# Kernel tuning notes

Hardware: AMD Instinct MI355X
Metric: run time of the kernel (lower is better)

The kernel has to match this reference:

```python
import jax, jax.numpy as jnp
import numpy as np

SIGMA = 100.0
M = 64
N_DIMS = 3
XH_IN = 9           # n_dims + in_node_nf + context_node_nf
XH_HID = 64         # xh_hidden_size
POS_HID = 192       # hidden_size - xh_hidden_size
TWO_PI = 2.0 * np.pi


def setup_inputs() -> dict:
    key = jax.random.key(0)
    ks = jax.random.split(key, 6)
    B, N = 8, 256
    t = jax.random.uniform(ks[0], (B, 1), dtype=jnp.float32)
    xh = jax.random.normal(ks[1], (B, N, XH_IN), dtype=jnp.float32)
    node_mask = jnp.ones((B, N, 1), dtype=jnp.float32)
    edge_mask = jnp.ones((B, N * N, 1), dtype=jnp.float32)
    # learned params: xh_embedder Linear(9->64), pos_embedder Linear(2m->192)
    W_xh = jax.random.normal(ks[2], (XH_IN, XH_HID), dtype=jnp.float32) / np.sqrt(XH_IN)
    b_xh = jnp.zeros((XH_HID,), dtype=jnp.float32)
    W_pos = jax.random.normal(ks[3], (2 * M, POS_HID), dtype=jnp.float32) / np.sqrt(2 * M)
    b_pos = jnp.zeros((POS_HID,), dtype=jnp.float32)
    return {"t": t, "xh": xh, "node_mask": node_mask, "edge_mask": edge_mask,
            "W_xh": W_xh, "b_xh": b_xh, "W_pos": W_pos, "b_pos": b_pos}


def remove_mean_with_mask(x, node_mask, N):
    # masked mean over node axis, re-masked output
    mean = jnp.sum(x * node_mask, axis=1, keepdims=True) / N  # [B,1,3]
    return (x - mean) * node_mask


def positional_encoding(d, sigma, m):
    # d: [B,N,N,1] -> Fourier features [B,N,N,2m] with geometric freqs sigma^(j/m)
    freqs = sigma ** (jnp.arange(m, dtype=jnp.float32) / m)  # [m]
    ang = TWO_PI * d * freqs                                  # [B,N,N,m]
    return jnp.concatenate([jnp.sin(ang), jnp.cos(ang)], axis=-1)


def reference(t, xh, node_mask, edge_mask, W_xh, b_xh, W_pos, b_pos):
    x = xh[..., :N_DIMS]
    h = xh[..., N_DIMS:]
    N = jnp.sum(node_mask, axis=1, keepdims=True)  # [B,1,1]
    x = remove_mean_with_mask(x, node_mask, N)
    # node feature embedding: [B,N,64]
    xh_emb = jnp.concatenate([x, h], axis=-1) @ W_xh + b_xh
    # pairwise distances (safe sqrt for diagonal zeros)
    diff = x[:, :, None, :] - x[:, None, :, :]                 # [B,N,N,3]
    sq = jnp.maximum(jnp.sum(diff * diff, axis=-1), 0.0)
    dist = jnp.sqrt(sq + 1e-12)                                # [B,N,N]
    pe = positional_encoding(dist[..., None], SIGMA, M)        # [B,N,N,2m]
    pe = pe * node_mask[:, :, :, None] * node_mask[:, None, :, :]
    pe = (pe @ W_pos + b_pos)                                  # [B,N,N,192]
    pe = jnp.sum(pe, axis=-2) / N                              # [B,N,192]
    out = jnp.concatenate([xh_emb, pe], axis=-1) * node_mask   # [B,N,256]
    return out
```

## Files before the change

### kernel.cpp

```cpp
#include <hip/hip_runtime.h>
#include <math.h>

#define BB 8
#define NN 256
#define XHIN 9
#define XHHID 64
#define POSHID 192

__global__ __launch_bounds__(256) void emb_center_kernel(
    const float* __restrict__ xh, const float* __restrict__ mask,
    const float* __restrict__ Wxh, const float* __restrict__ bxh,
    float* __restrict__ out, float* __restrict__ ws_xc, float* __restrict__ ws_cnt)
{
  const int b = blockIdx.x;
  const int n = threadIdx.x;

  const float* p = xh + (b * NN + n) * XHIN;
  float v[XHIN];
  #pragma unroll
  for (int k = 0; k < XHIN; ++k) v[k] = p[k];
  const float m = mask[b * NN + n];

  float a0 = v[0] * m, a1 = v[1] * m, a2 = v[2] * m, a3 = m;
  #pragma unroll
  for (int off = 32; off > 0; off >>= 1) {
    a0 += __shfl_down(a0, off, 64);
    a1 += __shfl_down(a1, off, 64);
    a2 += __shfl_down(a2, off, 64);
    a3 += __shfl_down(a3, off, 64);
  }
  __shared__ float red[4][4];
  __shared__ float Wl[XHIN * XHHID];
  __shared__ float bl[XHHID];
  const int lane = n & 63, wv = n >> 6;
  if (lane == 0) { red[wv][0] = a0; red[wv][1] = a1; red[wv][2] = a2; red[wv][3] = a3; }
  for (int idx = n; idx < XHIN * XHHID; idx += 256) Wl[idx] = Wxh[idx];
  if (n < XHHID) bl[n] = bxh[n];
  __syncthreads();

  const float s0 = red[0][0] + red[1][0] + red[2][0] + red[3][0];
  const float s1 = red[0][1] + red[1][1] + red[2][1] + red[3][1];
  const float s2 = red[0][2] + red[1][2] + red[2][2] + red[3][2];
  const float cnt = red[0][3] + red[1][3] + red[2][3] + red[3][3];
  const float inv = 1.0f / cnt;

  v[0] = (v[0] - s0 * inv) * m;
  v[1] = (v[1] - s1 * inv) * m;
  v[2] = (v[2] - s2 * inv) * m;

  ws_xc[(b * 3 + 0) * NN + n] = v[0];
  ws_xc[(b * 3 + 1) * NN + n] = v[1];
  ws_xc[(b * 3 + 2) * NN + n] = v[2];
  if (n == 0) ws_cnt[b] = cnt;

  float* o = out + (size_t)(b * NN + n) * 256;
  for (int oo = 0; oo < XHHID; ++oo) {
    float acc = bl[oo];
    #pragma unroll
    for (int k = 0; k < XHIN; ++k) acc = fmaf(v[k], Wl[k * XHHID + oo], acc);
    o[oo] = acc * m;
  }
}

__global__ __launch_bounds__(256) void pe_kernel(
    const float* __restrict__ ws_xc, const float* __restrict__ ws_cnt,
    const float* __restrict__ mask, const float* __restrict__ Wp,
    const float* __restrict__ bp, float* __restrict__ out)
{
  const int blk = blockIdx.x;
  const int b = blk >> 8;
  const int i = blk & 255;
  const int tid = threadIdx.x;

  __shared__ float dist_s[NN];
  __shared__ float mask_s[NN];
  __shared__ float part[4][128];
  __shared__ float Ssc[128];

  const float* xcb = ws_xc + b * 3 * NN;
  const float xi0 = xcb[0 * NN + i];
  const float xi1 = xcb[1 * NN + i];
  const float xi2 = xcb[2 * NN + i];
  {
    const int j = tid;
    const float dx = xi0 - xcb[0 * NN + j];
    const float dy = xi1 - xcb[1 * NN + j];
    const float dz = xi2 - xcb[2 * NN + j];
    const float sq = dx * dx + dy * dy + dz * dz;
    dist_s[j] = sqrtf(sq + 1e-12f);
    mask_s[j] = mask[b * NN + j];
  }
  __syncthreads();

  const int f = tid & 63, jg = tid >> 6;
  const float freq = (float)exp2((double)f * 0.10381025296523007);
  float ss = 0.f, cc = 0.f;
  const int j0 = jg * 64;
  #pragma unroll 16
  for (int u = 0; u < 64; ++u) {
    const float d = dist_s[j0 + u];
    const float mj = mask_s[j0 + u];
    const float r = d * freq;
    const float rv = r - floorf(r);
    ss = fmaf(__builtin_amdgcn_sinf(rv), mj, ss);
    cc = fmaf(__builtin_amdgcn_cosf(rv), mj, cc);
  }
  part[jg][f] = ss;
  part[jg][64 + f] = cc;
  __syncthreads();

  const float mi = mask[b * NN + i];
  const float cnt = ws_cnt[b];
  if (tid < 128) {
    const float s = part[0][tid] + part[1][tid] + part[2][tid] + part[3][tid];
    Ssc[tid] = s * (mi / cnt);
  }
  __syncthreads();

  if (tid < POSHID) {
    float acc = 0.f;
    #pragma unroll 8
    for (int k = 0; k < 128; ++k) acc = fmaf(Ssc[k], Wp[k * POSHID + tid], acc);
    acc += bp[tid] * (mi * 256.0f / cnt);
    out[(size_t)(b * NN + i) * 256 + 64 + tid] = acc;
  }
}

extern "C" void kernel_launch(void* const* d_in, const int* in_sizes, int n_in,
                              void* d_out, int out_size, void* d_ws, size_t ws_size,
                              hipStream_t stream) {
  const float* xh   = (const float*)d_in[1];
  const float* mask = (const float*)d_in[2];
  const float* Wxh  = (const float*)d_in[4];
  const float* bxh  = (const float*)d_in[5];
  const float* Wp   = (const float*)d_in[6];
  const float* bp   = (const float*)d_in[7];
  float* out = (float*)d_out;

  float* ws_xc  = (float*)d_ws;
  float* ws_cnt = ws_xc + BB * 3 * NN;

  emb_center_kernel<<<BB, 256, 0, stream>>>(xh, mask, Wxh, bxh, out, ws_xc, ws_cnt);
  pe_kernel<<<BB * NN, 256, 0, stream>>>(ws_xc, ws_cnt, mask, Wp, bp, out);
}
```

Before: 86.08 us.

## Move xh embedding into pe kernel and slim the centering kernel

Moves the 9->64 node embedding out of the 8-block centering kernel into the idle 64 threads of the per-node pe kernel, so the serial 8-block stage gets shorter and the embedding work is spread over all blocks. It also packs distance and mask into one float2 shared array, uses a hardware fract, computes the frequency with exp2f instead of double precision, and reads Ssc as float4. The single-precision exp2 may differ slightly from the double path. Both kernels now read xh.

```diff
diff --git a/kernel.cpp b/kernel.cpp
--- a/kernel.cpp
+++ b/kernel.cpp
@@ -7,21 +7,18 @@
 #define XHHID 64
 #define POSHID 192
 
-__global__ __launch_bounds__(256) void emb_center_kernel(
+__global__ __launch_bounds__(256) void mean_kernel(
     const float* __restrict__ xh, const float* __restrict__ mask,
-    const float* __restrict__ Wxh, const float* __restrict__ bxh,
-    float* __restrict__ out, float* __restrict__ ws_xc, float* __restrict__ ws_cnt)
+    float* __restrict__ ws_xc, float* __restrict__ ws_cnt)
 {
   const int b = blockIdx.x;
   const int n = threadIdx.x;
 
   const float* p = xh + (b * NN + n) * XHIN;
-  float v[XHIN];
-  #pragma unroll
-  for (int k = 0; k < XHIN; ++k) v[k] = p[k];
+  const float x0 = p[0], x1 = p[1], x2 = p[2];
   const float m = mask[b * NN + n];
 
-  float a0 = v[0] * m, a1 = v[1] * m, a2 = v[2] * m, a3 = m;
+  float a0 = x0 * m, a1 = x1 * m, a2 = x2 * m, a3 = m;
   #pragma unroll
   for (int off = 32; off > 0; off >>= 1) {
     a0 += __shfl_down(a0, off, 64);
@@ -30,12 +27,8 @@
     a3 += __shfl_down(a3, off, 64);
   }
   __shared__ float red[4][4];
-  __shared__ float Wl[XHIN * XHHID];
-  __shared__ float bl[XHHID];
   const int lane = n & 63, wv = n >> 6;
   if (lane == 0) { red[wv][0] = a0; red[wv][1] = a1; red[wv][2] = a2; red[wv][3] = a3; }
-  for (int idx = n; idx < XHIN * XHHID; idx += 256) Wl[idx] = Wxh[idx];
-  if (n < XHHID) bl[n] = bxh[n];
   __syncthreads();
 
   const float s0 = red[0][0] + red[1][0] + red[2][0] + red[3][0];
@@ -44,38 +37,28 @@
   const float cnt = red[0][3] + red[1][3] + red[2][3] + red[3][3];
   const float inv = 1.0f / cnt;
 
-  v[0] = (v[0] - s0 * inv) * m;
-  v[1] = (v[1] - s1 * inv) * m;
-  v[2] = (v[2] - s2 * inv) * m;
-
-  ws_xc[(b * 3 + 0) * NN + n] = v[0];
-  ws_xc[(b * 3 + 1) * NN + n] = v[1];
-  ws_xc[(b * 3 + 2) * NN + n] = v[2];
+  ws_xc[(b * 3 + 0) * NN + n] = (x0 - s0 * inv) * m;
+  ws_xc[(b * 3 + 1) * NN + n] = (x1 - s1 * inv) * m;
+  ws_xc[(b * 3 + 2) * NN + n] = (x2 - s2 * inv) * m;
   if (n == 0) ws_cnt[b] = cnt;
-
-  float* o = out + (size_t)(b * NN + n) * 256;
-  for (int oo = 0; oo < XHHID; ++oo) {
-    float acc = bl[oo];
-    #pragma unroll
-    for (int k = 0; k < XHIN; ++k) acc = fmaf(v[k], Wl[k * XHHID + oo], acc);
-    o[oo] = acc * m;
-  }
 }
 
 __global__ __launch_bounds__(256) void pe_kernel(
     const float* __restrict__ ws_xc, const float* __restrict__ ws_cnt,
-    const float* __restrict__ mask, const float* __restrict__ Wp,
-    const float* __restrict__ bp, float* __restrict__ out)
+    const float* __restrict__ mask, const float* __restrict__ xh,
+    const float* __restrict__ Wxh, const float* __restrict__ bxh,
+    const float* __restrict__ Wp, const float* __restrict__ bp,
+    float* __restrict__ out)
 {
   const int blk = blockIdx.x;
   const int b = blk >> 8;
   const int i = blk & 255;
   const int tid = threadIdx.x;
 
-  __shared__ float dist_s[NN];
-  __shared__ float mask_s[NN];
+  __shared__ float2 dm_s[NN];
   __shared__ float part[4][128];
-  __shared__ float Ssc[128];
+  __shared__ __align__(16) float Ssc[128];
+  __shared__ float ins_s[XHIN];
 
   const float* xcb = ws_xc + b * 3 * NN;
   const float xi0 = xcb[0 * NN + i];
@@ -86,43 +69,54 @@
     const float dx = xi0 - xcb[0 * NN + j];
     const float dy = xi1 - xcb[1 * NN + j];
     const float dz = xi2 - xcb[2 * NN + j];
-    const float sq = dx * dx + dy * dy + dz * dz;
-    dist_s[j] = sqrtf(sq + 1e-12f);
-    mask_s[j] = mask[b * NN + j];
+    const float sq = fmaf(dx, dx, fmaf(dy, dy, dz * dz));
+    dm_s[j] = make_float2(sqrtf(sq + 1e-12f), mask[b * NN + j]);
   }
+  if (tid < XHIN)
+    ins_s[tid] = (tid < 3) ? xcb[tid * NN + i] : xh[(b * NN + i) * XHIN + tid];
   __syncthreads();
 
   const int f = tid & 63, jg = tid >> 6;
-  const float freq = (float)exp2((double)f * 0.10381025296523007);
+  const float freq = __builtin_exp2f((float)f * 0.10381025296523007f);
   float ss = 0.f, cc = 0.f;
-  const int j0 = jg * 64;
+  const float2* dmp = dm_s + jg * 64;
   #pragma unroll 16
   for (int u = 0; u < 64; ++u) {
-    const float d = dist_s[j0 + u];
-    const float mj = mask_s[j0 + u];
-    const float r = d * freq;
-    const float rv = r - floorf(r);
-    ss = fmaf(__builtin_amdgcn_sinf(rv), mj, ss);
-    cc = fmaf(__builtin_amdgcn_cosf(rv), mj, cc);
+    const float2 dm = dmp[u];
+    const float rv = __builtin_amdgcn_fractf(dm.x * freq);
+    ss = fmaf(__builtin_amdgcn_sinf(rv), dm.y, ss);
+    cc = fmaf(__builtin_amdgcn_cosf(rv), dm.y, cc);
   }
   part[jg][f] = ss;
   part[jg][64 + f] = cc;
   __syncthreads();
 
-  const float mi = mask[b * NN + i];
   const float cnt = ws_cnt[b];
-  if (tid < 128) {
-    const float s = part[0][tid] + part[1][tid] + part[2][tid] + part[3][tid];
-    Ssc[tid] = s * (mi / cnt);
-  }
+  const float mi = dm_s[i].y;
+  if (tid < 128)
+    Ssc[tid] = (part[0][tid] + part[1][tid] + part[2][tid] + part[3][tid]) * (mi / cnt);
   __syncthreads();
 
   if (tid < POSHID) {
-    float acc = 0.f;
+    const float4* S4 = (const float4*)Ssc;
+    float acc = bp[tid] * (mi * 256.0f / cnt);
     #pragma unroll 8
-    for (int k = 0; k < 128; ++k) acc = fmaf(Ssc[k], Wp[k * POSHID + tid], acc);
-    acc += bp[tid] * (mi * 256.0f / cnt);
+    for (int k4 = 0; k4 < 32; ++k4) {
+      const float4 s = S4[k4];
+      const float* w = Wp + (k4 * 4) * POSHID + tid;
+      acc = fmaf(s.x, w[0 * POSHID], acc);
+      acc = fmaf(s.y, w[1 * POSHID], acc);
+      acc = fmaf(s.z, w[2 * POSHID], acc);
+      acc = fmaf(s.w, w[3 * POSHID], acc);
+    }
     out[(size_t)(b * NN + i) * 256 + 64 + tid] = acc;
+  } else {
+    const int oo = tid - POSHID;
+    float acc = bxh[oo];
+    #pragma unroll
+    for (int k = 0; k < XHIN; ++k)
+      acc = fmaf(ins_s[k], Wxh[k * XHHID + oo], acc);
+    out[(size_t)(b * NN + i) * 256 + oo] = acc * mi;
   }
 }
 
@@ -140,6 +134,6 @@
   float* ws_xc  = (float*)d_ws;
   float* ws_cnt = ws_xc + BB * 3 * NN;
 
-  emb_center_kernel<<<BB, 256, 0, stream>>>(xh, mask, Wxh, bxh, out, ws_xc, ws_cnt);
-  pe_kernel<<<BB * NN, 256, 0, stream>>>(ws_xc, ws_cnt, mask, Wp, bp, out);
+  mean_kernel<<<BB, 256, 0, stream>>>(xh, mask, ws_xc, ws_cnt);
+  pe_kernel<<<BB * NN, 256, 0, stream>>>(ws_xc, ws_cnt, mask, xh, Wxh, bxh, Wp, bp, out);
 }
```

Result: faster. 83.13 us (-3.4%).
